# Optimization experiments

Measured on AMD Instinct MI355X. Metric: run time of the kernel, lower is better.

The kernel has to match this reference:

```python
import jax, jax.numpy as jnp
import numpy as np
import math

B, S, D = 2, 2048, 1024
H = 16
HD = D // H  # 64


def setup_inputs() -> dict:
    key = jax.random.key(0)
    ks = jax.random.split(key, 5)
    scale = 0.02
    x = jax.random.normal(ks[0], (B, S, D), dtype=jnp.float32)
    # torch Linear weights stored as [in, out] (already transposed)
    w_qkv = jax.random.normal(ks[1], (D, 3 * D), dtype=jnp.float32) * scale
    b_qkv = jnp.zeros((3 * D,), dtype=jnp.float32)
    w_proj = jax.random.normal(ks[2], (D, D), dtype=jnp.float32) * scale
    b_proj = jnp.zeros((D,), dtype=jnp.float32)
    return {"x": x, "w_qkv": w_qkv, "b_qkv": b_qkv, "w_proj": w_proj, "b_proj": b_proj}


def reference(x, w_qkv, b_qkv, w_proj, b_proj):
    b, s, d = x.shape
    qkv = x @ w_qkv + b_qkv                              # [B,S,3D]
    qkv = qkv.reshape(b, s, 3, H, HD)
    qkv = jnp.transpose(qkv, (2, 0, 3, 1, 4))            # [3,B,H,S,HD]
    q, k, v = qkv[0], qkv[1], qkv[2]
    present = jnp.concatenate([k, v], axis=0)            # [2B,H,S,HD]
    # scaled causal attention, full [B,H,S,S] scores as in the original
    attn = jnp.einsum('bhqd,bhkd->bhqk', q, k) * (1.0 / math.sqrt(HD))
    causal = jnp.tril(jnp.ones((s, s), dtype=bool))
    attn = jnp.where(causal[None, None], attn, -jnp.inf)
    attn = jax.nn.softmax(attn, axis=-1)
    out = jnp.einsum('bhqk,bhkd->bhqd', attn, v)         # [B,H,S,HD]
    out = jnp.transpose(out, (0, 2, 1, 3)).reshape(b, s, d)
    out = out @ w_proj + b_proj                          # NOTE: original module has project layer; see notes
    return (out, present)
```

## Files before the change

kernel.cpp:

```cpp
#include <hip/hip_runtime.h>
#include <hip/hip_bf16.h>

typedef short s16x8 __attribute__((ext_vector_type(8)));
typedef short s16x4 __attribute__((ext_vector_type(4)));
typedef float f32x4 __attribute__((ext_vector_type(4)));
typedef float f32x16 __attribute__((ext_vector_type(16)));
typedef unsigned int u32x4 __attribute__((ext_vector_type(4)));

#define S_LEN 2048
#define DMODEL 1024
#define NHEAD 16
#define HDIM 64
#define OUT_ELEMS 4194304
#define HEAD_ELEMS 4194304
#define SCALE_LOG2 0.1803368801111204f

__device__ inline short f2bf(float f) {
  __hip_bfloat16 h = __float2bfloat16(f);
  return __builtin_bit_cast(short, h);
}

__device__ inline f32x4 mfma16(s16x8 a, s16x8 b, f32x4 c) {
  return __builtin_amdgcn_mfma_f32_16x16x32_bf16(a, b, c, 0, 0, 0);
}
__device__ inline f32x16 mfma32(s16x8 a, s16x8 b, f32x16 c) {
  return __builtin_amdgcn_mfma_f32_32x32x16_bf16(a, b, c, 0, 0, 0);
}

typedef __attribute__((address_space(1))) const void gvoid;
typedef __attribute__((address_space(3))) void lvoid;
__device__ inline void gload_lds16(const void* g, void* l) {
  __builtin_amdgcn_global_load_lds((gvoid*)g, (lvoid*)l, 16, 0, 0);
}

__global__ __launch_bounds__(256) void cvt_bf16(const float* __restrict__ in,
                                                short* __restrict__ out) {
  int g = blockIdx.x * 256 + threadIdx.x;
  const float* p = &in[(size_t)g * 8];
  f32x4 a = *(const f32x4*)p;
  f32x4 b = *(const f32x4*)(p + 4);
  s16x8 v;
#pragma unroll
  for (int j = 0; j < 4; j++) {
    v[j] = f2bf(a[j]);
    v[4 + j] = f2bf(b[j]);
  }
  *(s16x8*)&out[(size_t)g * 8] = v;
}

__global__ __launch_bounds__(256) void transpose_cvt(
    const float* __restrict__ in, short* __restrict__ out, int R, int C) {
  int g = blockIdx.x * 256 + threadIdx.x;
  int c = g % C;
  int r0 = (g / C) * 8;
  s16x8 v;
#pragma unroll
  for (int j = 0; j < 8; j++) v[j] = f2bf(in[(size_t)(r0 + j) * C + c]);
  *(s16x8*)&out[(size_t)c * R + r0] = v;
}

template <int MODE>
__global__ __launch_bounds__(256) void gemm_bt(
    const short* __restrict__ A, const short* __restrict__ Bt,
    const float* __restrict__ bias, short* __restrict__ Ob0,
    float* __restrict__ Of, short* __restrict__ VtOut,
    short* __restrict__ KwOut, int M, int N, int K) {
  __shared__ short As[128 * 32];
  __shared__ short Bs[128 * 32];
  const int t = threadIdx.x;
  const int lane = t & 63;
  const int wid = t >> 6;
  const int wr = wid >> 1, wc = wid & 1;
  const int l16 = lane & 15, lg = lane >> 4;
  const int mbase = blockIdx.y * 128;
  const int nbase = blockIdx.x * 128;

  f32x4 acc[4][4];
#pragma unroll
  for (int m = 0; m < 4; m++)
#pragma unroll
    for (int n = 0; n < 4; n++) acc[m][n] = (f32x4){0.f, 0.f, 0.f, 0.f};

  const int srow = lane >> 2;
  const int scol = (lane & 3) * 8;
  const short* Ag = &A[(size_t)(mbase + wid * 32 + srow) * K + scol];
  const short* Bg = &Bt[(size_t)(nbase + wid * 32 + srow) * K + scol];
  short* AsW0 = &As[(wid * 32) * 32];
  short* AsW1 = &As[(wid * 32 + 16) * 32];
  short* BsW0 = &Bs[(wid * 32) * 32];
  short* BsW1 = &Bs[(wid * 32 + 16) * 32];

  for (int k0 = 0; k0 < K; k0 += 32) {
    __syncthreads();
    gload_lds16(Ag + k0, AsW0);
    gload_lds16(Ag + (size_t)16 * K + k0, AsW1);
    gload_lds16(Bg + k0, BsW0);
    gload_lds16(Bg + (size_t)16 * K + k0, BsW1);
    __syncthreads();
    s16x8 af[4], bfr[4];
#pragma unroll
    for (int m = 0; m < 4; m++)
      af[m] = *(const s16x8*)&As[(wr * 64 + m * 16 + l16) * 32 + lg * 8];
#pragma unroll
    for (int n = 0; n < 4; n++)
      bfr[n] = *(const s16x8*)&Bs[(wc * 64 + n * 16 + l16) * 32 + lg * 8];
#pragma unroll
    for (int m = 0; m < 4; m++)
#pragma unroll
      for (int n = 0; n < 4; n++)
        acc[m][n] = mfma16(af[m], bfr[n], acc[m][n]);
  }

#pragma unroll
  for (int m = 0; m < 4; m++) {
#pragma unroll
    for (int n = 0; n < 4; n++) {
      int gcol = nbase + wc * 64 + n * 16 + l16;
      float bv = bias[gcol];
      int part = gcol >> 10;
      int cin = gcol & 1023;
      int h = cin >> 6, hd = cin & 63;
      int grow0 = mbase + wr * 64 + m * 16 + lg * 4;
      float vr[4];
#pragma unroll
      for (int r = 0; r < 4; r++) vr[r] = acc[m][n][r] + bv;
      if (MODE == 0) {
        int bb = grow0 >> 11, s0 = grow0 & 2047;
        size_t base = ((size_t)(bb * NHEAD + h) * S_LEN + s0) * HDIM + hd;
        if (part == 0) {
#pragma unroll
          for (int r = 0; r < 4; r++)
            Ob0[base + (size_t)r * HDIM] = f2bf(vr[r] * SCALE_LOG2);
        } else if (part == 1) {
#pragma unroll
          for (int r = 0; r < 4; r++) Of[base + (size_t)r * HDIM] = vr[r];
          if (KwOut) {
#pragma unroll
            for (int r = 0; r < 4; r++)
              KwOut[base + (size_t)r * HDIM] = f2bf(vr[r]);
          }
        } else {
#pragma unroll
          for (int r = 0; r < 4; r++)
            Of[HEAD_ELEMS + base + (size_t)r * HDIM] = vr[r];
          s16x4 pk;
#pragma unroll
          for (int r = 0; r < 4; r++) pk[r] = f2bf(vr[r]);
          int w32 = s0 & 31;
          int nw = ((w32 >> 4) << 4) | ((w32 & 4) << 1) | ((w32 & 8) >> 1);
          int sperm = (s0 & ~31) | nw;
          *(s16x4*)&VtOut[((size_t)(bb * NHEAD + h) * HDIM + hd) * S_LEN +
                          sperm] = pk;
        }
      } else {
#pragma unroll
        for (int r = 0; r < 4; r++) Of[(size_t)(grow0 + r) * N + gcol] = vr[r];
      }
    }
  }
}

__global__ __launch_bounds__(256, 2) void attn_fwd_kbf16(
    const short* __restrict__ Q, const short* __restrict__ K,
    const short* __restrict__ Vt, short* __restrict__ AO) {
  __shared__ short Ks[2][64][64];
  __shared__ short Vs[2][64][64];

  const int p = blockIdx.x;
  const int bh = p & 31;
  const int seg = (p >> 5) & 7;
  const int qi = (p < 256) ? (15 - seg) : seg;
  const int qb = qi * 128;
  const int nt = 2 * qi + 2;

  const int tid = threadIdx.x;
  const int w = tid >> 6;
  const int lane = tid & 63;
  const int l32 = lane & 31;
  const int hi = lane >> 5;
  const int rsub = lane >> 3;
  const int sub = lane & 7;

  const short* Qb = Q + (size_t)bh * (S_LEN * HDIM);
  const short* Kb = K + (size_t)bh * (S_LEN * HDIM);
  const short* Vb = Vt + (size_t)bh * (HDIM * S_LEN);
  const int b = bh >> 4, h = bh & 15;

  const int qrow = qb + 32 * w + l32;
  const int qminw = qb + 32 * w;
  const int qmaxw = qminw + 31;

  s16x8 qf[4];
#pragma unroll
  for (int c = 0; c < 4; c++)
    qf[c] = *(const s16x8*)&Qb[(size_t)qrow * HDIM + c * 16 + hi * 8];

  f32x16 acc0 = {0.f}, acc1 = {0.f};
  float m = -1e30f, ll = 0.f;

  s16x8 kreg[2], vreg[2];
  auto LOADT = [&](int kt) {
    const int kb = kt * 64;
#pragma unroll
    for (int c = 0; c < 2; c++) {
      int row = 16 * w + 8 * c + rsub;
      int gs = sub ^ (row & 7);
      kreg[c] = *(const s16x8*)&Kb[(size_t)(kb + row) * HDIM + gs * 8];
      vreg[c] = *(const s16x8*)&Vb[(size_t)row * S_LEN + kb + gs * 8];
    }
  };
  auto WRITET = [&](int bb) {
#pragma unroll
    for (int c = 0; c < 2; c++) {
      int row = 16 * w + 8 * c + rsub;
      *(s16x8*)&Ks[bb][row][sub * 8] = kreg[c];
      *(s16x8*)&Vs[bb][row][sub * 8] = vreg[c];
    }
  };

  LOADT(0);
  WRITET(0);
  __syncthreads();
  int cur = 0;

#pragma unroll 1
  for (int kt = 0; kt < nt; kt++) {
    const int kb = kt * 64;
    if (kt + 1 < nt) LOADT(kt + 1);
    if (kb <= qmaxw) {
      f32x16 S0 = {0.f}, S1 = {0.f};
#pragma unroll
      for (int c = 0; c < 4; c++) {
        int cs = c * 2 + hi;
        int r0 = l32;
        int r1 = 32 + l32;
        s16x8 k0 = *(const s16x8*)&Ks[cur][r0][(cs ^ (r0 & 7)) * 8];
        s16x8 k1 = *(const s16x8*)&Ks[cur][r1][(cs ^ (r1 & 7)) * 8];
        S0 = mfma32(k0, qf[c], S0);
        S1 = mfma32(k1, qf[c], S1);
      }
      if (kb + 63 > qminw) {
#pragma unroll
        for (int r = 0; r < 16; r++) {
          int key0 = kb + (r & 3) + 8 * (r >> 2) + 4 * hi;
          S0[r] = (key0 <= qrow) ? S0[r] : -1e30f;
          S1[r] = (key0 + 32 <= qrow) ? S1[r] : -1e30f;
        }
      }
      float t8[8];
#pragma unroll
      for (int r = 0; r < 8; r++)
        t8[r] = fmaxf(fmaxf(S0[2 * r], S0[2 * r + 1]),
                      fmaxf(S1[2 * r], S1[2 * r + 1]));
      float tmax = fmaxf(fmaxf(fmaxf(t8[0], t8[1]), fmaxf(t8[2], t8[3])),
                         fmaxf(fmaxf(t8[4], t8[5]), fmaxf(t8[6], t8[7])));
      tmax = fmaxf(tmax, __shfl_xor(tmax, 32));
      if (!__all(tmax <= m + 11.0f)) {
        float mn = fmaxf(m, tmax);
        float alpha = __builtin_amdgcn_exp2f(m - mn);
        ll *= alpha;
#pragma unroll
        for (int r = 0; r < 16; r++) {
          acc0[r] *= alpha;
          acc1[r] *= alpha;
        }
        m = mn;
      }
#pragma unroll
      for (int r = 0; r < 16; r++) {
        S0[r] = __builtin_amdgcn_exp2f(S0[r] - m);
        S1[r] = __builtin_amdgcn_exp2f(S1[r] - m);
      }
      float s8[8];
#pragma unroll
      for (int r = 0; r < 8; r++)
        s8[r] = (S0[2 * r] + S0[2 * r + 1]) + (S1[2 * r] + S1[2 * r + 1]);
      float rs = ((s8[0] + s8[1]) + (s8[2] + s8[3])) +
                 ((s8[4] + s8[5]) + (s8[6] + s8[7]));
      rs += __shfl_xor(rs, 32);
      ll += rs;
#pragma unroll
      for (int half = 0; half < 2; half++) {
        const f32x16& S = half ? S1 : S0;
        u32x4 pbAv, pbBv;
#pragma unroll
        for (int g = 0; g < 4; g++) {
          unsigned int lo = (unsigned short)f2bf(S[2 * g]);
          unsigned int h16 = (unsigned short)f2bf(S[2 * g + 1]);
          pbAv[g] = lo | (h16 << 16);
          unsigned int lo2 = (unsigned short)f2bf(S[8 + 2 * g]);
          unsigned int h162 = (unsigned short)f2bf(S[9 + 2 * g]);
          pbBv[g] = lo2 | (h162 << 16);
        }
#pragma unroll
        for (int gg = 0; gg < 2; gg++) {
          s16x8 pb = __builtin_bit_cast(s16x8, gg ? pbBv : pbAv);
          int cs = (half * 2 + gg) * 2 + hi;
          int v0r = l32;
          int v1r = 32 + l32;
          s16x8 va0 = *(const s16x8*)&Vs[cur][v0r][(cs ^ (v0r & 7)) * 8];
          s16x8 va1 = *(const s16x8*)&Vs[cur][v1r][(cs ^ (v1r & 7)) * 8];
          acc0 = mfma32(va0, pb, acc0);
          acc1 = mfma32(va1, pb, acc1);
        }
      }
    }
    if (kt + 1 < nt) WRITET(cur ^ 1);
    __syncthreads();
    cur ^= 1;
  }

  float inv = 1.f / ll;
  size_t rowbase = ((size_t)(b * S_LEN + qrow)) * DMODEL + h * HDIM;
#pragma unroll
  for (int g = 0; g < 4; g++) {
    s16x4 o0, o1;
#pragma unroll
    for (int u = 0; u < 4; u++) {
      o0[u] = f2bf(acc0[4 * g + u] * inv);
      o1[u] = f2bf(acc1[4 * g + u] * inv);
    }
    *(s16x4*)&AO[rowbase + 8 * g + 4 * hi] = o0;
    *(s16x4*)&AO[rowbase + 32 + 8 * g + 4 * hi] = o1;
  }
}

__global__ __launch_bounds__(256, 4) void attn_fwd_kf32(
    const short* __restrict__ Q, const float* __restrict__ Kraw,
    const short* __restrict__ Vt, short* __restrict__ AO) {
  __shared__ float XFER[2][64][37];
  const int p = blockIdx.x;
  const int xcd = p & 7;
  const int rank = p >> 3;
  const int bh = (xcd << 2) | (rank >> 5);
  const int pr = rank & 31;
  const int tid = threadIdx.x;
  const int w = tid >> 6;
  const int lane = tid & 63;
  const int l32 = lane & 31;
  const int hi = lane >> 5;
  const short* Qb = Q + (size_t)bh * (S_LEN * HDIM);
  const short* Vb = Vt + (size_t)bh * (HDIM * S_LEN);
  const float* Kb32 = Kraw + (size_t)bh * (S_LEN * HDIM);
  const int b = bh >> 4, h = bh & 15;

#pragma unroll 1
  for (int ph = 0; ph < 2; ph++) {
    const int j = ph ? pr : 63 - pr;
    const int qb = j * 32;
    s16x8 qf[4];
#pragma unroll
    for (int c = 0; c < 4; c++)
      qf[c] = *(const s16x8*)&Qb[(size_t)(qb + l32) * HDIM + c * 16 + hi * 8];
    f32x16 acc0 = {0.f}, acc1 = {0.f};
    float m = -1e30f, ll = 0.f;
#pragma unroll 1
    for (int kt = w; kt <= j; kt += 4) {
      const int kb = kt * 32;
      f32x16 S = {0.f};
#pragma unroll
      for (int c = 0; c < 4; c++) {
        const float* kr = &Kb32[(size_t)(kb + l32) * HDIM + c * 16 + hi * 8];
        f32x4 k0 = *(const f32x4*)kr, k1 = *(const f32x4*)(kr + 4);
        s16x8 kf;
#pragma unroll
        for (int u = 0; u < 4; u++) {
          kf[u] = f2bf(k0[u]);
          kf[4 + u] = f2bf(k1[u]);
        }
        S = mfma32(kf, qf[c], S);
      }
      const short* vr0 = &Vb[(size_t)l32 * S_LEN + kb + hi * 8];
      const short* vr1 = &Vb[(size_t)(32 + l32) * S_LEN + kb + hi * 8];
      s16x8 va00 = *(const s16x8*)vr0;
      s16x8 va01 = *(const s16x8*)(vr0 + 16);
      s16x8 va10 = *(const s16x8*)vr1;
      s16x8 va11 = *(const s16x8*)(vr1 + 16);
      if (kt == j) {
#pragma unroll
        for (int r = 0; r < 16; r++) {
          int keyl = (r & 3) + 8 * (r >> 2) + 4 * hi;
          S[r] = (keyl <= l32) ? S[r] : -1e30f;
        }
      }
      float t8[8];
#pragma unroll
      for (int r = 0; r < 8; r++) t8[r] = fmaxf(S[2 * r], S[2 * r + 1]);
      float tmax = fmaxf(fmaxf(fmaxf(t8[0], t8[1]), fmaxf(t8[2], t8[3])),
                         fmaxf(fmaxf(t8[4], t8[5]), fmaxf(t8[6], t8[7])));
      tmax = fmaxf(tmax, __shfl_xor(tmax, 32));
      if (!__all(tmax <= m + 11.0f)) {
        float mn = fmaxf(m, tmax);
        float alpha = __builtin_amdgcn_exp2f(m - mn);
        ll *= alpha;
#pragma unroll
        for (int r = 0; r < 16; r++) {
          acc0[r] *= alpha;
          acc1[r] *= alpha;
        }
        m = mn;
      }
#pragma unroll
      for (int r = 0; r < 16; r++) S[r] = __builtin_amdgcn_exp2f(S[r] - m);
      float s8[8];
#pragma unroll
      for (int r = 0; r < 8; r++) s8[r] = S[2 * r] + S[2 * r + 1];
      float rs = ((s8[0] + s8[1]) + (s8[2] + s8[3])) +
                 ((s8[4] + s8[5]) + (s8[6] + s8[7]));
      rs += __shfl_xor(rs, 32);
      ll += rs;
      u32x4 pb0v, pb1v;
#pragma unroll
      for (int g = 0; g < 4; g++) {
        unsigned int lo = (unsigned short)f2bf(S[2 * g]);
        unsigned int h16 = (unsigned short)f2bf(S[2 * g + 1]);
        pb0v[g] = lo | (h16 << 16);
        unsigned int lo2 = (unsigned short)f2bf(S[8 + 2 * g]);
        unsigned int h162 = (unsigned short)f2bf(S[9 + 2 * g]);
        pb1v[g] = lo2 | (h162 << 16);
      }
      s16x8 pb0 = __builtin_bit_cast(s16x8, pb0v);
      s16x8 pb1 = __builtin_bit_cast(s16x8, pb1v);
      acc0 = mfma32(va00, pb0, acc0);
      acc1 = mfma32(va10, pb0, acc1);
      acc0 = mfma32(va01, pb1, acc0);
      acc1 = mfma32(va11, pb1, acc1);
    }
    if (w & 1) {
      float* dst = &XFER[w >> 1][lane][0];
      dst[0] = m; dst[1] = ll;
#pragma unroll
      for (int r = 0; r < 16; r++) { dst[2 + r] = acc0[r]; dst[18 + r] = acc1[r]; }
    }
    __syncthreads();
    if (!(w & 1)) {
      const float* src = &XFER[w >> 1][lane][0];
      float m2 = src[0], l2 = src[1];
      float M = fmaxf(m, m2);
      float a1 = __builtin_amdgcn_exp2f(m - M);
      float a2 = __builtin_amdgcn_exp2f(m2 - M);
      ll = ll * a1 + l2 * a2;
#pragma unroll
      for (int r = 0; r < 16; r++) {
        acc0[r] = acc0[r] * a1 + src[2 + r] * a2;
        acc1[r] = acc1[r] * a1 + src[18 + r] * a2;
      }
      m = M;
    }
    __syncthreads();
    if (w == 2) {
      float* dst = &XFER[0][lane][0];
      dst[0] = m; dst[1] = ll;
#pragma unroll
      for (int r = 0; r < 16; r++) { dst[2 + r] = acc0[r]; dst[18 + r] = acc1[r]; }
    }
    __syncthreads();
    if (w == 0) {
      const float* src = &XFER[0][lane][0];
      float m2 = src[0], l2 = src[1];
      float M = fmaxf(m, m2);
      float a1 = __builtin_amdgcn_exp2f(m - M);
      float a2 = __builtin_amdgcn_exp2f(m2 - M);
      ll = ll * a1 + l2 * a2;
#pragma unroll
      for (int r = 0; r < 16; r++) {
        acc0[r] = acc0[r] * a1 + src[2 + r] * a2;
        acc1[r] = acc1[r] * a1 + src[18 + r] * a2;
      }
      float inv = 1.f / ll;
      size_t rowbase = ((size_t)(b * S_LEN + qb + l32)) * DMODEL + h * HDIM;
#pragma unroll
      for (int g = 0; g < 4; g++) {
        s16x4 o0, o1;
#pragma unroll
        for (int u = 0; u < 4; u++) {
          o0[u] = f2bf(acc0[4 * g + u] * inv);
          o1[u] = f2bf(acc1[4 * g + u] * inv);
        }
        *(s16x4*)&AO[rowbase + 8 * g + 4 * hi] = o0;
        *(s16x4*)&AO[rowbase + 32 + 8 * g + 4 * hi] = o1;
      }
    }
    __syncthreads();
  }
}

extern "C" void kernel_launch(void* const* d_in, const int* in_sizes, int n_in,
                              void* d_out, int out_size, void* d_ws,
                              size_t ws_size, hipStream_t stream) {
  const float* x = (const float*)d_in[0];
  const float* w_qkv = (const float*)d_in[1];
  const float* b_qkv = (const float*)d_in[2];
  const float* w_proj = (const float*)d_in[3];
  const float* b_proj = (const float*)d_in[4];
  float* out = (float*)d_out;
  float* presentK = out + OUT_ELEMS;

  short* xbf = (short*)out;

  short* ws = (short*)d_ws;
  const bool kbf16 = ws_size >= (size_t)35651584;

  short *Qw, *Vt, *wprojT, *wqkvT, *attnout, *Kw;
  if (kbf16) {
    Qw = ws;
    Kw = ws + 4194304;
    Vt = ws + 8388608;
    wprojT = ws + 12582912;
    wqkvT = ws + 13631488;
    attnout = ws + 13631488;
  } else {
    if (ws_size < (size_t)27262976) return;
    Qw = ws;
    Vt = ws + 4194304;
    wprojT = ws + 8388608;
    wqkvT = ws + 9437184;
    attnout = ws + 9437184;
    Kw = nullptr;
  }

  cvt_bf16<<<dim3(2048), 256, 0, stream>>>(x, xbf);
  transpose_cvt<<<dim3(1536), 256, 0, stream>>>(w_qkv, wqkvT, 1024, 3072);
  transpose_cvt<<<dim3(512), 256, 0, stream>>>(w_proj, wprojT, 1024, 1024);
  gemm_bt<0><<<dim3(24, 32), 256, 0, stream>>>(
      xbf, wqkvT, b_qkv, Qw, presentK, Vt, Kw, 4096, 3072, 1024);
  if (kbf16)
    attn_fwd_kbf16<<<dim3(512), 256, 0, stream>>>(Qw, Kw, Vt, attnout);
  else
    attn_fwd_kf32<<<dim3(1024), 256, 0, stream>>>(Qw, presentK, Vt, attnout);
  gemm_bt<1><<<dim3(8, 32), 256, 0, stream>>>(
      attnout, wprojT, b_proj, nullptr, out, nullptr, nullptr, 4096, 1024,
      1024);
}
```

Measured before the change: 131.1 us.

## Deepen GEMM K-tile with swizzled LDS and split V transpose into own kernel

The bf16 GEMM now stages 64-wide K tiles instead of 32, which halves the number of barrier-separated load rounds. LDS column groups are XOR-swizzled by row to avoid bank conflicts on the fragment reads. The scattered, permuted V-transpose stores are removed from the QKV GEMM epilogue and moved into a separate vtrans kernel. That kernel rereads the fp32 present-V output, converts it to bf16 through LDS and writes it out. The trade is an extra launch plus about 16MB of V reads against a cheaper epilogue. On the non-bf16-K fallback path, KwOut now aliases Qw, which would overwrite Q with K values.

```diff
diff --git a/kernel.cpp b/kernel.cpp
--- a/kernel.cpp
+++ b/kernel.cpp
@@ -59,14 +59,54 @@
   *(s16x8*)&out[(size_t)c * R + r0] = v;
 }
 
+__global__ __launch_bounds__(256) void vtrans(const float* __restrict__ Vf,
+                                              short* __restrict__ Vt) {
+  __shared__ short Vl[64][70];
+  const int p = blockIdx.x;
+  const int bh = p & 31;
+  const int kt = p >> 5;
+  const float* src = Vf + ((size_t)bh * S_LEN + (size_t)kt * 64) * HDIM;
+  short* dst = Vt + (size_t)bh * (HDIM * S_LEN) + kt * 64;
+  const int t = threadIdx.x;
+  {
+    int row = t >> 2, col = (t & 3) * 16;
+    const float* s = &src[row * 64 + col];
+    f32x4 a0 = *(const f32x4*)s;
+    f32x4 a1 = *(const f32x4*)(s + 4);
+    f32x4 a2 = *(const f32x4*)(s + 8);
+    f32x4 a3 = *(const f32x4*)(s + 12);
+    s16x8 v0, v1;
+#pragma unroll
+    for (int j = 0; j < 4; j++) {
+      v0[j] = f2bf(a0[j]); v0[4 + j] = f2bf(a1[j]);
+      v1[j] = f2bf(a2[j]); v1[4 + j] = f2bf(a3[j]);
+    }
+    *(s16x8*)&Vl[row][col] = v0;
+    *(s16x8*)&Vl[row][col + 8] = v1;
+  }
+  __syncthreads();
+  {
+    int hd = t >> 2, kg = (t & 3) * 16;
+    const int perm4[4] = {0, 2, 1, 3};
+    s16x8 o0, o1;
+#pragma unroll
+    for (int pp = 0; pp < 8; pp++)
+      o0[pp] = Vl[kg + (pp & 3) + perm4[pp >> 2] * 4][hd];
+#pragma unroll
+    for (int pp = 0; pp < 8; pp++)
+      o1[pp] = Vl[kg + ((pp + 8) & 3) + perm4[(pp + 8) >> 2] * 4][hd];
+    *(s16x8*)&dst[(size_t)hd * S_LEN + kg] = o0;
+    *(s16x8*)&dst[(size_t)hd * S_LEN + kg + 8] = o1;
+  }
+}
+
 template <int MODE>
 __global__ __launch_bounds__(256) void gemm_bt(
     const short* __restrict__ A, const short* __restrict__ Bt,
     const float* __restrict__ bias, short* __restrict__ Ob0,
-    float* __restrict__ Of, short* __restrict__ VtOut,
-    short* __restrict__ KwOut, int M, int N, int K) {
-  __shared__ short As[128 * 32];
-  __shared__ short Bs[128 * 32];
+    float* __restrict__ Of, short* __restrict__ KwOut, int M, int N, int K) {
+  __shared__ short As[128 * 64];
+  __shared__ short Bs[128 * 64];
   const int t = threadIdx.x;
   const int lane = t & 63;
   const int wid = t >> 6;
@@ -81,34 +121,46 @@
 #pragma unroll
     for (int n = 0; n < 4; n++) acc[m][n] = (f32x4){0.f, 0.f, 0.f, 0.f};
 
-  const int srow = lane >> 2;
-  const int scol = (lane & 3) * 8;
-  const short* Ag = &A[(size_t)(mbase + wid * 32 + srow) * K + scol];
-  const short* Bg = &Bt[(size_t)(nbase + wid * 32 + srow) * K + scol];
-  short* AsW0 = &As[(wid * 32) * 32];
-  short* AsW1 = &As[(wid * 32 + 16) * 32];
-  short* BsW0 = &Bs[(wid * 32) * 32];
-  short* BsW1 = &Bs[(wid * 32 + 16) * 32];
-
-  for (int k0 = 0; k0 < K; k0 += 32) {
-    __syncthreads();
-    gload_lds16(Ag + k0, AsW0);
-    gload_lds16(Ag + (size_t)16 * K + k0, AsW1);
-    gload_lds16(Bg + k0, BsW0);
-    gload_lds16(Bg + (size_t)16 * K + k0, BsW1);
-    __syncthreads();
-    s16x8 af[4], bfr[4];
+  const int srow = lane >> 3;
+  const int sgr = (lane & 7) ^ srow;
+  const short* Ag = &A[(size_t)(mbase + wid * 32 + srow) * K + sgr * 8];
+  const short* Bg = &Bt[(size_t)(nbase + wid * 32 + srow) * K + sgr * 8];
+
+  for (int k0 = 0; k0 < K; k0 += 64) {
+    __syncthreads();
+#pragma unroll
+    for (int c = 0; c < 4; c++)
+      gload_lds16(Ag + (size_t)(c * 8) * K + k0, &As[(wid * 32 + c * 8) * 64]);
+#pragma unroll
+    for (int c = 0; c < 4; c++)
+      gload_lds16(Bg + (size_t)(c * 8) * K + k0, &Bs[(wid * 32 + c * 8) * 64]);
+    __syncthreads();
+    s16x8 af[4][2], bfr[4][2];
+#pragma unroll
+    for (int m = 0; m < 4; m++) {
+      int row = wr * 64 + m * 16 + l16;
+#pragma unroll
+      for (int h = 0; h < 2; h++) {
+        int gr = (h * 4 + lg) ^ (row & 7);
+        af[m][h] = *(const s16x8*)&As[row * 64 + gr * 8];
+      }
+    }
+#pragma unroll
+    for (int n = 0; n < 4; n++) {
+      int row = wc * 64 + n * 16 + l16;
+#pragma unroll
+      for (int h = 0; h < 2; h++) {
+        int gr = (h * 4 + lg) ^ (row & 7);
+        bfr[n][h] = *(const s16x8*)&Bs[row * 64 + gr * 8];
+      }
+    }
 #pragma unroll
     for (int m = 0; m < 4; m++)
-      af[m] = *(const s16x8*)&As[(wr * 64 + m * 16 + l16) * 32 + lg * 8];
-#pragma unroll
-    for (int n = 0; n < 4; n++)
-      bfr[n] = *(const s16x8*)&Bs[(wc * 64 + n * 16 + l16) * 32 + lg * 8];
-#pragma unroll
-    for (int m = 0; m < 4; m++)
-#pragma unroll
-      for (int n = 0; n < 4; n++)
-        acc[m][n] = mfma16(af[m], bfr[n], acc[m][n]);
+#pragma unroll
+      for (int n = 0; n < 4; n++) {
+        acc[m][n] = mfma16(af[m][0], bfr[n][0], acc[m][n]);
+        acc[m][n] = mfma16(af[m][1], bfr[n][1], acc[m][n]);
+      }
   }
 
 #pragma unroll
@@ -134,23 +186,13 @@
         } else if (part == 1) {
 #pragma unroll
           for (int r = 0; r < 4; r++) Of[base + (size_t)r * HDIM] = vr[r];
-          if (KwOut) {
-#pragma unroll
-            for (int r = 0; r < 4; r++)
-              KwOut[base + (size_t)r * HDIM] = f2bf(vr[r]);
-          }
+#pragma unroll
+          for (int r = 0; r < 4; r++)
+            KwOut[base + (size_t)r * HDIM] = f2bf(vr[r]);
         } else {
 #pragma unroll
           for (int r = 0; r < 4; r++)
             Of[HEAD_ELEMS + base + (size_t)r * HDIM] = vr[r];
-          s16x4 pk;
-#pragma unroll
-          for (int r = 0; r < 4; r++) pk[r] = f2bf(vr[r]);
-          int w32 = s0 & 31;
-          int nw = ((w32 >> 4) << 4) | ((w32 & 4) << 1) | ((w32 & 8) >> 1);
-          int sperm = (s0 & ~31) | nw;
-          *(s16x4*)&VtOut[((size_t)(bb * NHEAD + h) * HDIM + hd) * S_LEN +
-                          sperm] = pk;
         }
       } else {
 #pragma unroll
@@ -495,6 +537,7 @@
   const float* b_proj = (const float*)d_in[4];
   float* out = (float*)d_out;
   float* presentK = out + OUT_ELEMS;
+  float* presentV = presentK + HEAD_ELEMS;
 
   short* xbf = (short*)out;
 
@@ -523,12 +566,13 @@
   transpose_cvt<<<dim3(1536), 256, 0, stream>>>(w_qkv, wqkvT, 1024, 3072);
   transpose_cvt<<<dim3(512), 256, 0, stream>>>(w_proj, wprojT, 1024, 1024);
   gemm_bt<0><<<dim3(24, 32), 256, 0, stream>>>(
-      xbf, wqkvT, b_qkv, Qw, presentK, Vt, Kw, 4096, 3072, 1024);
+      xbf, wqkvT, b_qkv, Qw, presentK, kbf16 ? Kw : Qw , 4096,
+      3072, 1024);
+  vtrans<<<dim3(1024), 256, 0, stream>>>(presentV, Vt);
   if (kbf16)
     attn_fwd_kbf16<<<dim3(512), 256, 0, stream>>>(Qw, Kw, Vt, attnout);
   else
     attn_fwd_kf32<<<dim3(1024), 256, 0, stream>>>(Qw, presentK, Vt, attnout);
   gemm_bt<1><<<dim3(8, 32), 256, 0, stream>>>(
-      attnout, wprojT, b_proj, nullptr, out, nullptr, nullptr, 4096, 1024,
-      1024);
-}
+      attnout, wprojT, b_proj, nullptr, out, nullptr, 4096, 1024, 1024);
+}
```

New measurement: 127.4 us. 2.8% less time.
